# Kernel tuning notes

Hardware: AMD Instinct MI355X
Metric: run time of the kernel (lower is better)

The kernel has to match this reference:

```python
import jax, jax.numpy as jnp
import numpy as np

GAMMA = 2.0
CONTEXT_WINDOW = 100


def setup_inputs() -> dict:
    key = jax.random.key(0)
    k1, k2 = jax.random.split(key)
    B, S, C = 64, 131072, 3
    inputs = jax.random.normal(k1, (B, S, C), dtype=jnp.float32)
    targets = jax.random.randint(k2, (B, S), 0, C, dtype=jnp.int32)
    alpha = jnp.array([0.25, 1.0, 1.0], dtype=jnp.float32)
    return {"inputs": inputs, "targets": targets, "alpha": alpha}


def _window_mask(targets, window):
    # mask[b, i] = True iff any positive target within +/- window of i;
    # rows with no positives are fully True (matches torch loop semantics).
    B, S = targets.shape
    pos = targets > 0                                   # (B, S) bool
    cs = jnp.cumsum(pos.astype(jnp.int32), axis=1)      # inclusive prefix sums
    c = jnp.concatenate([jnp.zeros((B, 1), jnp.int32), cs], axis=1)  # (B, S+1)
    idx = jnp.arange(S)
    hi = jnp.minimum(idx + window + 1, S)               # exclusive end
    lo = jnp.maximum(idx - window, 0)                   # inclusive start
    count = c[:, hi] - c[:, lo]                         # positives in window
    mask = count > 0
    has_pos = pos.any(axis=1, keepdims=True)
    return jnp.where(has_pos, mask, True)


def reference(inputs, targets, alpha):
    # inputs: (B, S, C) logits; targets: (B, S) class indices
    mask = _window_mask(targets, CONTEXT_WINDOW)                     # (B, S)
    logp = jax.nn.log_softmax(inputs, axis=-1)                       # (B, S, C)
    ce = -jnp.take_along_axis(logp, targets[..., None].astype(jnp.int32), axis=-1)[..., 0]
    p_t = jnp.exp(-ce)
    focal = alpha[targets] * (1.0 - p_t) ** GAMMA * ce               # (B, S)
    m = mask.astype(inputs.dtype)
    # masked mean == mean over selected elements in the torch version
    return jnp.sum(focal * m) / jnp.sum(m)
```

## Files before the change

### kernel.cpp

```cpp
#include <hip/hip_runtime.h>

#define BB 64
#define SS 131072
#define WIN 100
#define TILE 2048
#define NTHREADS 256
#define NBLOCKS (BB * (SS / TILE))
#define EXT (TILE + 2*WIN)
#define NITER ((EXT + NTHREADS - 1) / NTHREADS)
#define NWORDS ((EXT + 63) / 64)

__global__ __launch_bounds__(NTHREADS) void focal_main(
    const float* __restrict__ inputs, const int* __restrict__ targets,
    const float* __restrict__ alpha, double* __restrict__ slots)
{
    __shared__ unsigned char sh_t[EXT];
    __shared__ unsigned long long wbits[NWORDS];
    __shared__ double red[(NTHREADS/64) * 4];

    const int t = threadIdx.x;
    const int b = blockIdx.x >> 6;
    const int tile = blockIdx.x & 63;
    const int s0 = tile * TILE;
    const int ext_lo = (s0 - WIN > 0) ? (s0 - WIN) : 0;
    const int ext_hi = (s0 + TILE + WIN < SS) ? (s0 + TILE + WIN) : SS;
    const int ext_len = ext_hi - ext_lo;

    const float* inrow = inputs + (long)b * SS * 3;
    const int p0 = s0 + t * 4;
    const int p1 = s0 + (NTHREADS + t) * 4;
    const float4* ip0 = (const float4*)(inrow + (long)p0 * 3);
    const float4* ip1 = (const float4*)(inrow + (long)p1 * 3);
    const float4 q0 = ip0[0], q1 = ip0[1], q2 = ip0[2];
    const float4 q3 = ip1[0], q4 = ip1[1], q5 = ip1[2];

    const int* trow = targets + (long)b * SS;
    int tvv[NITER];
    #pragma unroll
    for (int it = 0; it < NITER; ++it) {
        const int k = it * NTHREADS + t;
        tvv[it] = (k < ext_len) ? trow[ext_lo + k] : 0;
    }
    const int wave = t >> 6, lane = t & 63;
    #pragma unroll
    for (int it = 0; it < NITER; ++it) {
        const int k = it * NTHREADS + t;
        if (k < ext_len) sh_t[k] = (unsigned char)tvv[it];
        const unsigned long long bal = __ballot(tvv[it] > 0);
        if (lane == 0) wbits[it * 4 + wave] = bal;
    }
    __syncthreads();

    const float a0 = alpha[0], a1 = alpha[1], a2 = alpha[2];
    float fsum_m = 0.0f, fsum_a = 0.0f;
    int cnt_m = 0, cnt_p = 0;

    const float xs[24] = {q0.x, q0.y, q0.z, q0.w, q1.x, q1.y, q1.z, q1.w,
                          q2.x, q2.y, q2.z, q2.w, q3.x, q3.y, q3.z, q3.w,
                          q4.x, q4.y, q4.z, q4.w, q5.x, q5.y, q5.z, q5.w};

    #pragma unroll
    for (int g = 0; g < 2; ++g) {
        const int p = (g == 0) ? p0 : p1;
        #pragma unroll
        for (int j = 0; j < 4; ++j) {
            const int i = p + j;
            const float x0 = xs[g*12 + 3*j], x1 = xs[g*12 + 3*j + 1],
                        x2 = xs[g*12 + 3*j + 2];
            const int tv = sh_t[i - ext_lo];
            const float mx = fmaxf(x0, fmaxf(x1, x2));
            const float e0 = __expf(x0 - mx), e1 = __expf(x1 - mx), e2 = __expf(x2 - mx);
            const float lse = mx + __logf(e0 + e1 + e2);
            const float xt = (tv == 0) ? x0 : ((tv == 1) ? x1 : x2);
            const float ce = lse - xt;
            const float pt = __expf(-ce);
            const float w  = (tv == 0) ? a0 : ((tv == 1) ? a1 : a2);
            const float om = 1.0f - pt;
            const float focal = w * om * om * ce;

            int glo = i - WIN; if (glo < 0) glo = 0;
            int ghi = i + WIN; if (ghi > SS - 1) ghi = SS - 1;
            const int jlo = glo - ext_lo, jhi = ghi - ext_lo;
            const int w0 = jlo >> 6, w1 = jhi >> 6;
            unsigned long long acc = 0;
            for (int wd = w0; wd <= w1; ++wd) {
                unsigned long long v = wbits[wd];
                if (wd == w0) v &= (~0ULL) << (jlo & 63);
                if (wd == w1) v &= (~0ULL) >> (63 - (jhi & 63));
                acc |= v;
            }
            const bool m = (acc != 0);

            fsum_a += focal;
            fsum_m += m ? focal : 0.0f;
            cnt_m += m ? 1 : 0;
            cnt_p += (tv > 0) ? 1 : 0;
        }
    }

    double dm = (double)fsum_m, da = (double)fsum_a;
    double dc = (double)cnt_m, dp = (double)cnt_p;
    #pragma unroll
    for (int off = 32; off >= 1; off >>= 1) {
        dm += __shfl_down(dm, off);
        da += __shfl_down(da, off);
        dc += __shfl_down(dc, off);
        dp += __shfl_down(dp, off);
    }
    if (lane == 0) {
        red[wave*4]   = dm; red[wave*4+1] = dc;
        red[wave*4+2] = da; red[wave*4+3] = dp;
    }
    __syncthreads();
    if (t == 0) {
        double sm = 0, sc = 0, sa = 0, sp = 0;
        #pragma unroll
        for (int w = 0; w < NTHREADS/64; ++w) {
            sm += red[w*4]; sc += red[w*4+1]; sa += red[w*4+2]; sp += red[w*4+3];
        }
        double* slot = slots + (long)blockIdx.x * 4;
        slot[0] = sm;
        slot[1] = sc;
        slot[2] = sa;
        slot[3] = sp;
    }
}

__global__ __launch_bounds__(NTHREADS) void focal_final(
    const double* __restrict__ slots, float* __restrict__ out)
{
    __shared__ double red[(NTHREADS/64) * 2];
    __shared__ double tot[2];
    const int t = threadIdx.x;
    const int wave = t >> 6, lane = t & 63;

    double sm = 0.0, sc = 0.0;
    for (int k = t; k < NBLOCKS; k += NTHREADS) {
        sm += slots[(long)k * 4 + 0];
        sc += slots[(long)k * 4 + 1];
    }
    #pragma unroll
    for (int off = 32; off >= 1; off >>= 1) {
        sm += __shfl_down(sm, off);
        sc += __shfl_down(sc, off);
    }
    if (lane == 0) { red[wave*2] = sm; red[wave*2+1] = sc; }
    __syncthreads();
    if (t == 0) {
        double a = 0, b = 0;
        #pragma unroll
        for (int w = 0; w < NTHREADS/64; ++w) { a += red[w*2]; b += red[w*2+1]; }
        tot[0] = a; tot[1] = b;
    }
    __syncthreads();

    double corr_s = 0.0, corr_c = 0.0;
    if (t < BB) {
        double row_sum = 0.0, row_pos = 0.0;
        for (int j = 0; j < 64; ++j) {
            const long blk = (long)t * 64 + j;
            row_sum += slots[blk * 4 + 2];
            row_pos += slots[blk * 4 + 3];
        }
        if (row_pos == 0.0) { corr_s = row_sum; corr_c = (double)SS; }
    }
    if (wave == 0) {
        #pragma unroll
        for (int off = 32; off >= 1; off >>= 1) {
            corr_s += __shfl_down(corr_s, off);
            corr_c += __shfl_down(corr_c, off);
        }
        if (t == 0) {
            const double total = tot[0] + corr_s;
            const double count = tot[1] + corr_c;
            out[0] = (float)(total / count);
        }
    }
}

extern "C" void kernel_launch(void* const* d_in, const int* in_sizes, int n_in,
                              void* d_out, int out_size, void* d_ws, size_t ws_size,
                              hipStream_t stream) {
    const float* inputs  = (const float*)d_in[0];
    const int*   targets = (const int*)d_in[1];
    const float* alpha   = (const float*)d_in[2];
    float* out = (float*)d_out;

    double* slots = (double*)d_ws;

    focal_main<<<NBLOCKS, NTHREADS, 0, stream>>>(inputs, targets, alpha, slots);
    focal_final<<<1, NTHREADS, 0, stream>>>(slots, out);
}
```

Before: 184.2 us.

## Precompute window mask via bitwise dilation with wave shuffles

Replaces the per-element loop over ballot words with a one-time dilation of the positive-target bitmask across the tile, using shifts and neighbour-word shuffles so each element reads one mask bit. Also derives p_t from the softmax ratio instead of a second exp, loads four targets as one packed word, counts positives during the load, and reduces partial sums in float/int before converting to double. The cost is a short extra pass and barrier done by one wave, plus some loss of reduction precision within each wave.

```diff
diff --git a/kernel.cpp b/kernel.cpp
--- a/kernel.cpp
+++ b/kernel.cpp
@@ -16,6 +16,7 @@
 {
     __shared__ unsigned char sh_t[EXT];
     __shared__ unsigned long long wbits[NWORDS];
+    __shared__ unsigned long long mbits[NWORDS];
     __shared__ double red[(NTHREADS/64) * 4];
 
     const int t = threadIdx.x;
@@ -35,25 +36,40 @@
     const float4 q3 = ip1[0], q4 = ip1[1], q5 = ip1[2];
 
     const int* trow = targets + (long)b * SS;
-    int tvv[NITER];
+    const int wave = t >> 6, lane = t & 63;
+    const int tr_lo = s0 - ext_lo;
+    int cnt_p = 0;
     #pragma unroll
     for (int it = 0; it < NITER; ++it) {
         const int k = it * NTHREADS + t;
-        tvv[it] = (k < ext_len) ? trow[ext_lo + k] : 0;
+        const int tv = (k < ext_len) ? trow[ext_lo + k] : 0;
+        if (k < ext_len) sh_t[k] = (unsigned char)tv;
+        const bool pos = (tv > 0);
+        cnt_p += (pos && k >= tr_lo && k < tr_lo + TILE) ? 1 : 0;
+        const unsigned long long bal = __ballot(pos);
+        if (lane == 0) wbits[it * 4 + wave] = bal;
     }
-    const int wave = t >> 6, lane = t & 63;
-    #pragma unroll
-    for (int it = 0; it < NITER; ++it) {
-        const int k = it * NTHREADS + t;
-        if (k < ext_len) sh_t[k] = (unsigned char)tvv[it];
-        const unsigned long long bal = __ballot(tvv[it] > 0);
-        if (lane == 0) wbits[it * 4 + wave] = bal;
+    __syncthreads();
+
+    if (wave == 0) {
+        unsigned long long x = (lane < NWORDS) ? wbits[lane] : 0ULL;
+        const int shifts[7] = {1, 2, 4, 8, 16, 32, 37};
+        #pragma unroll
+        for (int s_i = 0; s_i < 7; ++s_i) {
+            const int s = shifts[s_i];
+            unsigned long long up = __shfl_up(x, 1);
+            if (lane == 0) up = 0ULL;
+            unsigned long long dn = __shfl_down(x, 1);
+            if (lane == 63) dn = 0ULL;
+            x = x | (x << s) | (up >> (64 - s)) | (x >> s) | (dn << (64 - s));
+        }
+        if (lane < NWORDS) mbits[lane] = x;
     }
     __syncthreads();
 
     const float a0 = alpha[0], a1 = alpha[1], a2 = alpha[2];
     float fsum_m = 0.0f, fsum_a = 0.0f;
-    int cnt_m = 0, cnt_p = 0;
+    int cnt_m = 0;
 
     const float xs[24] = {q0.x, q0.y, q0.z, q0.w, q1.x, q1.y, q1.z, q1.w,
                           q2.x, q2.y, q2.z, q2.w, q3.x, q3.y, q3.z, q3.w,
@@ -62,54 +78,42 @@
     #pragma unroll
     for (int g = 0; g < 2; ++g) {
         const int p = (g == 0) ? p0 : p1;
+        const int j0 = p - ext_lo;
+        const unsigned long long mw = mbits[j0 >> 6];
+        const unsigned int tpack = *(const unsigned int*)(sh_t + j0);
         #pragma unroll
         for (int j = 0; j < 4; ++j) {
-            const int i = p + j;
             const float x0 = xs[g*12 + 3*j], x1 = xs[g*12 + 3*j + 1],
                         x2 = xs[g*12 + 3*j + 2];
-            const int tv = sh_t[i - ext_lo];
+            const int tv = (tpack >> (8 * j)) & 0xFF;
             const float mx = fmaxf(x0, fmaxf(x1, x2));
             const float e0 = __expf(x0 - mx), e1 = __expf(x1 - mx), e2 = __expf(x2 - mx);
-            const float lse = mx + __logf(e0 + e1 + e2);
-            const float xt = (tv == 0) ? x0 : ((tv == 1) ? x1 : x2);
-            const float ce = lse - xt;
-            const float pt = __expf(-ce);
-            const float w  = (tv == 0) ? a0 : ((tv == 1) ? a1 : a2);
-            const float om = 1.0f - pt;
+            const float sum = e0 + e1 + e2;
+            const float xt  = (tv == 0) ? x0 : ((tv == 1) ? x1 : x2);
+            const float et  = (tv == 0) ? e0 : ((tv == 1) ? e1 : e2);
+            const float ce  = __logf(sum) + (mx - xt);
+            const float pt  = et * __frcp_rn(sum);
+            const float w   = (tv == 0) ? a0 : ((tv == 1) ? a1 : a2);
+            const float om  = 1.0f - pt;
             const float focal = w * om * om * ce;
-
-            int glo = i - WIN; if (glo < 0) glo = 0;
-            int ghi = i + WIN; if (ghi > SS - 1) ghi = SS - 1;
-            const int jlo = glo - ext_lo, jhi = ghi - ext_lo;
-            const int w0 = jlo >> 6, w1 = jhi >> 6;
-            unsigned long long acc = 0;
-            for (int wd = w0; wd <= w1; ++wd) {
-                unsigned long long v = wbits[wd];
-                if (wd == w0) v &= (~0ULL) << (jlo & 63);
-                if (wd == w1) v &= (~0ULL) >> (63 - (jhi & 63));
-                acc |= v;
-            }
-            const bool m = (acc != 0);
+            const bool  m   = (mw >> ((j0 & 63) + j)) & 1ULL;
 
             fsum_a += focal;
             fsum_m += m ? focal : 0.0f;
-            cnt_m += m ? 1 : 0;
-            cnt_p += (tv > 0) ? 1 : 0;
+            cnt_m  += m ? 1 : 0;
         }
     }
 
-    double dm = (double)fsum_m, da = (double)fsum_a;
-    double dc = (double)cnt_m, dp = (double)cnt_p;
     #pragma unroll
     for (int off = 32; off >= 1; off >>= 1) {
-        dm += __shfl_down(dm, off);
-        da += __shfl_down(da, off);
-        dc += __shfl_down(dc, off);
-        dp += __shfl_down(dp, off);
+        fsum_m += __shfl_down(fsum_m, off);
+        fsum_a += __shfl_down(fsum_a, off);
+        cnt_m  += __shfl_down(cnt_m, off);
+        cnt_p  += __shfl_down(cnt_p, off);
     }
     if (lane == 0) {
-        red[wave*4]   = dm; red[wave*4+1] = dc;
-        red[wave*4+2] = da; red[wave*4+3] = dp;
+        red[wave*4]   = (double)fsum_m; red[wave*4+1] = (double)cnt_m;
+        red[wave*4+2] = (double)fsum_a; red[wave*4+3] = (double)cnt_p;
     }
     __syncthreads();
     if (t == 0) {
```

Measured after the change: 190.5 us. 3.5% more time.
